# Kernel optimization log

Hardware: AMD Instinct MI355X
Metric: run time of the kernel (lower is better)

Reference implementation:

```python
import jax, jax.numpy as jnp
import numpy as np

DIV = 8

def setup_inputs() -> dict:
    key = jax.random.key(0)
    x = jax.random.uniform(key, (32, 3, 1024, 1024), dtype=jnp.float32)
    return {"x": x}

def reference(x):
    b, c, h, w = x.shape
    bh, bw = h // DIV, w // DIV
    # [b, 3, DIV, bh, DIV, bw] -> per-block stats over (bh, bw)
    xb = x.reshape(b, c, DIV, bh, DIV, bw)
    mean = xb.mean(axis=(3, 5))          # [b, 3, DIV, DIV]
    mx = xb.max(axis=(3, 5))
    mn = xb.min(axis=(3, 5))

    def pair_term(i, j):
        # skip (contribute 0) iff min_i > max_j or max_i < min_j
        skip = (mn[:, i] > mx[:, j]) | (mx[:, i] < mn[:, j])
        d = (mean[:, i] - mean[:, j]) ** 2
        return jnp.where(skip, 0.0, d)

    D = pair_term(0, 1) + pair_term(1, 2) + pair_term(0, 2)  # [b, DIV, DIV]
    k = D.sum() / (DIV * DIV)
    return k.reshape(1)
```

## Files before the change

kernel.cpp:

```cpp
#include <hip/hip_runtime.h>

#define DIVN 8
#define NB 32
#define NC 3
#define NIMG (NB * NC)
#define NBLK (NIMG * DIVN * DIVN)
#define ROWS_PER_CHUNK 64
#define NCHUNK (NIMG * 16)

typedef float floatx4 __attribute__((ext_vector_type(4)));

__global__ __launch_bounds__(256) void stats_kernel(
    const float* __restrict__ x,
    double* __restrict__ wsum,
    float* __restrict__ wmn,
    float* __restrict__ wmx) {
    const int ch  = blockIdx.x;
    const int tid = threadIdx.x;
    const float* base = x + (size_t)ch * (ROWS_PER_CHUNK * 1024) + tid * 4;

    double s = 0.0;
    float mn = 3.402823466e38f;
    float mx = -3.402823466e38f;

    #pragma unroll 8
    for (int i = 0; i < ROWS_PER_CHUNK; ++i) {
        const floatx4 v = __builtin_nontemporal_load(
            reinterpret_cast<const floatx4*>(base + (size_t)i * 1024));
        const float ps = (v.x + v.y) + (v.z + v.w);
        s += (double)ps;
        mn = fminf(mn, fminf(fminf(v.x, v.y), fminf(v.z, v.w)));
        mx = fmaxf(mx, fmaxf(fmaxf(v.x, v.y), fmaxf(v.z, v.w)));
    }

    for (int off = 16; off > 0; off >>= 1) {
        s  += __shfl_down(s, off, 32);
        mn  = fminf(mn, __shfl_down(mn, off, 32));
        mx  = fmaxf(mx, __shfl_down(mx, off, 32));
    }

    if ((tid & 31) == 0) {
        const int bj   = tid >> 5;
        const int half = ch & 1;
        const int bi   = (ch >> 1) & 7;
        const int img  = ch >> 4;
        const int g    = img * 64 + bi * 8 + bj;
        wsum[half * NBLK + g] = s;
        wmn [half * NBLK + g] = mn;
        wmx [half * NBLK + g] = mx;
    }
}

__global__ __launch_bounds__(256) void pair_reduce_kernel(
    const double* __restrict__ wsum,
    const float* __restrict__ wmn,
    const float* __restrict__ wmx,
    float* __restrict__ out) {
    const int tid = threadIdx.x;
    double acc = 0.0;

    for (int item = tid; item < NB * DIVN * DIVN; item += 256) {
        const int p = item & 63;
        const int b = item >> 6;
        float m[3], n[3], X[3];
        #pragma unroll
        for (int c = 0; c < 3; ++c) {
            const int i = (b * 3 + c) * 64 + p;
            m[c] = (float)((wsum[i] + wsum[NBLK + i]) * (1.0 / 16384.0));
            n[c] = fminf(wmn[i], wmn[NBLK + i]);
            X[c] = fmaxf(wmx[i], wmx[NBLK + i]);
        }
        if (!((n[0] > X[1]) || (X[0] < n[1]))) { const float d = m[0] - m[1]; acc += (double)(d * d); }
        if (!((n[1] > X[2]) || (X[1] < n[2]))) { const float d = m[1] - m[2]; acc += (double)(d * d); }
        if (!((n[0] > X[2]) || (X[0] < n[2]))) { const float d = m[0] - m[2]; acc += (double)(d * d); }
    }

    __shared__ double sacc[256];
    sacc[tid] = acc;
    __syncthreads();
    for (int off = 128; off > 0; off >>= 1) {
        if (tid < off) sacc[tid] += sacc[tid + off];
        __syncthreads();
    }
    if (tid == 0) out[0] = (float)(sacc[0] * (1.0 / (DIVN * DIVN)));
}

extern "C" void kernel_launch(void* const* d_in, const int* in_sizes, int n_in,
                              void* d_out, int out_size, void* d_ws, size_t ws_size,
                              hipStream_t stream) {
    const float* x = (const float*)d_in[0];
    float* out = (float*)d_out;

    double* wsum = (double*)d_ws;
    float*  wmn  = (float*)(wsum + 2 * NBLK);
    float*  wmx  = wmn + 2 * NBLK;

    stats_kernel<<<NCHUNK, 256, 0, stream>>>(x, wsum, wmn, wmx);
    pair_reduce_kernel<<<1, 256, 0, stream>>>(wsum, wmn, wmx, out);
}
```

Measured before the change: 69.03 us.

## Stream input rows through LDS with async global_load_lds multi-buffering

Replaces the per-thread nontemporal register loads with global_load_lds DMA into a four-slot LDS ring, keeping three rows in flight per wave and waiting on vmcnt before each row is consumed. The goal is deeper memory-level parallelism to better saturate HBM bandwidth in a streaming reduction. It adds LDS traffic and manual waitcnt handling, and drops the nontemporal hint. Each wave only reads back its own LDS slot, so no barrier is used; correctness depends on the waitcnt ordering.

After: 79.96 us. 1.16x slower.

```diff
diff --git a/kernel.cpp b/kernel.cpp
--- a/kernel.cpp
+++ b/kernel.cpp
@@ -2,36 +2,57 @@
 
 #define DIVN 8
 #define NB 32
-#define NC 3
-#define NIMG (NB * NC)
-#define NBLK (NIMG * DIVN * DIVN)
-#define ROWS_PER_CHUNK 64
-#define NCHUNK (NIMG * 16)
+#define NBLK 6144
+#define NCHUNK 1536
 
 typedef float floatx4 __attribute__((ext_vector_type(4)));
+
+__device__ __forceinline__ void gll16(const void* g, void* l) {
+    __builtin_amdgcn_global_load_lds(
+        (const __attribute__((address_space(1))) void*)g,
+        (__attribute__((address_space(3))) void*)l, 16, 0, 0);
+}
 
 __global__ __launch_bounds__(256) void stats_kernel(
     const float* __restrict__ x,
     double* __restrict__ wsum,
     float* __restrict__ wmn,
     float* __restrict__ wmx) {
+    __shared__ floatx4 lds[4][4][64];
     const int ch  = blockIdx.x;
     const int tid = threadIdx.x;
-    const float* base = x + (size_t)ch * (ROWS_PER_CHUNK * 1024) + tid * 4;
+    const int w   = tid >> 6;
+    const int l   = tid & 63;
+
+    const char* g0 = (const char*)x + (size_t)ch * (64 * 4096) + w * 1024 + l * 16;
 
     double s = 0.0;
     float mn = 3.402823466e38f;
     float mx = -3.402823466e38f;
 
-    #pragma unroll 8
-    for (int i = 0; i < ROWS_PER_CHUNK; ++i) {
-        const floatx4 v = __builtin_nontemporal_load(
-            reinterpret_cast<const floatx4*>(base + (size_t)i * 1024));
-        const float ps = (v.x + v.y) + (v.z + v.w);
-        s += (double)ps;
-        mn = fminf(mn, fminf(fminf(v.x, v.y), fminf(v.z, v.w)));
-        mx = fmaxf(mx, fmaxf(fmaxf(v.x, v.y), fmaxf(v.z, v.w)));
+    gll16(g0,            &lds[0][w][0]);
+    gll16(g0 + 4096,     &lds[1][w][0]);
+    gll16(g0 + 2 * 4096, &lds[2][w][0]);
+
+#define CONSUME(i) do {                                              \
+        const floatx4 v = lds[(i) & 3][w][l];                        \
+        s += (double)((v.x + v.y) + (v.z + v.w));                    \
+        mn = fminf(mn, fminf(fminf(v.x, v.y), fminf(v.z, v.w)));     \
+        mx = fmaxf(mx, fmaxf(fmaxf(v.x, v.y), fmaxf(v.z, v.w)));     \
+    } while (0)
+
+    for (int i = 0; i < 61; ++i) {
+        gll16(g0 + (size_t)(i + 3) * 4096, &lds[(i + 3) & 3][w][0]);
+        asm volatile("s_waitcnt vmcnt(3)" ::: "memory");
+        CONSUME(i);
     }
+    asm volatile("s_waitcnt vmcnt(2)" ::: "memory");
+    CONSUME(61);
+    asm volatile("s_waitcnt vmcnt(1)" ::: "memory");
+    CONSUME(62);
+    asm volatile("s_waitcnt vmcnt(0)" ::: "memory");
+    CONSUME(63);
+#undef CONSUME
 
     for (int off = 16; off > 0; off >>= 1) {
         s  += __shfl_down(s, off, 32);
```
